# Kernel optimization log

Hardware: AMD Instinct MI355X
Metric: run time of the kernel (lower is better)

Reference implementation:

```python
import jax, jax.numpy as jnp
import numpy as np

B, N, NIN, NHID, D = 8, 2048, 256, 256, 64  # head = 1 (required by squeeze())


def setup_inputs() -> dict:
    key = jax.random.key(0)
    ks = jax.random.split(key, 12)
    xn = lambda k, shape, s=1.0: jax.random.normal(k, shape, jnp.float32) * s
    xav = lambda fi, fo: (2.0 / (fi + fo)) ** 0.5  # xavier_normal std
    return {
        "inputs": xn(ks[0], (B, N, NIN)),
        "fc1_w": xn(ks[1], (NHID, NIN), xav(NIN, NHID)),
        "fc1_b": jnp.full((NHID,), 0.1, jnp.float32),
        "fc2_w": xn(ks[2], (NHID, NHID), xav(NHID, NHID)),
        "fc2_b": jnp.full((NHID,), 0.1, jnp.float32),
        "bn_g": 1.0 + 0.1 * xn(ks[3], (NHID,)),
        "bn_b": 0.1 * xn(ks[4], (NHID,)),
        "bn_mean": 0.1 * xn(ks[5], (NHID,)),
        "bn_var": jax.random.uniform(ks[6], (NHID,), jnp.float32, 0.5, 1.5),
        "wq_w": xn(ks[7], (D, NHID), xav(NHID, D)),
        "wq_b": jnp.full((D,), 0.1, jnp.float32),
        "wk_w": xn(ks[8], (D, NHID), xav(NHID, D)),
        "wk_b": jnp.full((D,), 0.1, jnp.float32),
        "mlp2_w": xn(ks[9], (1, 2 * D), xav(2 * D, 1)),
        "mlp2_b": jnp.full((1,), 0.1, jnp.float32),
    }


def reference(inputs, fc1_w, fc1_b, fc2_w, fc2_b, bn_g, bn_b, bn_mean, bn_var,
              wq_w, wq_b, wk_w, wk_b, mlp2_w, mlp2_b):
    # MLP: Linear -> ELU -> (dropout off, eval) -> Linear -> ELU -> BatchNorm1d (eval, running stats)
    x = jax.nn.elu(jnp.einsum('bni,hi->bnh', inputs, fc1_w) + fc1_b)
    x = jax.nn.elu(jnp.einsum('bnh,oh->bno', x, fc2_w) + fc2_b)
    X = (x - bn_mean) * jax.lax.rsqrt(bn_var + 1e-5) * bn_g + bn_b  # [B,N,NHID]
    # Q/K projections (head=1 -> shapes [B,N,D])
    Xq = jnp.einsum('bnh,dh->bnd', X, wq_w) + wq_b
    Xk = jnp.einsum('bnh,dh->bnd', X, wk_w) + wk_b
    # Original: cat([NK, NQ], -1) over all (i,j) pairs then Linear(2D -> 1).
    # Algebraically identical decomposition: probs[b,i,j] = Xk[b,j].wk_half + Xq[b,i].wq_half + bias
    wk_half, wq_half = mlp2_w[0, :D], mlp2_w[0, D:]
    sk = Xk @ wk_half  # [B,N]  (varies with j, the K/column index)
    sq = Xq @ wq_half  # [B,N]  (varies with i, the Q/row index)
    probs = sq[:, :, None] + sk[:, None, :] + mlp2_b[0]  # [B,N,N]
    return probs
```

## Files before the change

kernel.cpp:

```cpp
#include <hip/hip_runtime.h>
#include <hip/hip_bf16.h>
#include <math.h>

typedef __bf16 bf16x8 __attribute__((ext_vector_type(8)));
typedef float  f32x4  __attribute__((ext_vector_type(4)));
typedef unsigned int u32;
typedef u32 u32x4 __attribute__((ext_vector_type(4)));
typedef unsigned short u16;

#define WS_STG1  0
#define WS_STG2  32768
#define WS_UQ    65536
#define WS_UK    65792
#define WS_CONST 66048
#define WS_SQ    66064
#define WS_SK    82448

__device__ __forceinline__ float elu1(float x) {
    return x > 0.f ? x : (__expf(x) - 1.f);
}

__global__ void prep_all(const float* __restrict__ w1, const float* __restrict__ w2,
                         const float* __restrict__ bn_g, const float* __restrict__ bn_b,
                         const float* __restrict__ bn_mean, const float* __restrict__ bn_var,
                         const float* __restrict__ wq_w, const float* __restrict__ wq_b,
                         const float* __restrict__ wk_w, const float* __restrict__ wk_b,
                         const float* __restrict__ mlp2_w, const float* __restrict__ mlp2_b,
                         float* __restrict__ ws) {
    if (blockIdx.x == 0) {
        __shared__ float redq[256], redk[256];
        const int h = threadIdx.x;
        float s  = bn_g[h] * rsqrtf(bn_var[h] + 1e-5f);
        float tt = bn_b[h] - bn_mean[h] * s;
        float vq = 0.f, vk = 0.f;
        #pragma unroll
        for (int d = 0; d < 64; ++d) {
            vq += wq_w[d * 256 + h] * mlp2_w[64 + d];
            vk += wk_w[d * 256 + h] * mlp2_w[d];
        }
        ws[WS_UQ + h] = s * vq;
        ws[WS_UK + h] = s * vk;
        redq[h] = tt * vq;
        redk[h] = tt * vk;
        __syncthreads();
        for (int st = 128; st > 0; st >>= 1) {
            if (h < st) { redq[h] += redq[h + st]; redk[h] += redk[h + st]; }
            __syncthreads();
        }
        if (h == 0) {
            float cq = 0.f, ck = 0.f;
            for (int d = 0; d < 64; ++d) {
                cq += wq_b[d] * mlp2_w[64 + d];
                ck += wk_b[d] * mlp2_w[d];
            }
            ws[WS_CONST + 0] = redq[0] + cq;
            ws[WS_CONST + 1] = redk[0] + ck;
            ws[WS_CONST + 2] = mlp2_b[0];
        }
        return;
    }
    const int bid = blockIdx.x - 1;
    const int m   = bid >> 3;
    const int kt  = bid & 7;
    const float* src = m ? w2 : w1;
    __bf16* stg = (__bf16*)(ws + (m ? WS_STG2 : WS_STG1));
    const int tid = threadIdx.x;
    #pragma unroll
    for (int it = 0; it < 4; ++it) {
        int idx = it * 256 + tid;
        int nt = idx >> 6, l = idx & 63;
        int lr = l & 15, lk = l >> 4;
        const float* sp = src + (nt * 16 + lr) * 256 + kt * 32 + lk * 8;
        bf16x8 hi;
        #pragma unroll
        for (int j = 0; j < 8; ++j) hi[j] = (__bf16)sp[j];
        *(bf16x8*)(stg + (kt * 16 + nt) * 512 + l * 8) = hi;
    }
}

__global__ __launch_bounds__(256) void main_mfma(const float* __restrict__ inp,
                                                 const float* __restrict__ b1,
                                                 const float* __restrict__ b2,
                                                 float* __restrict__ ws) {
    __shared__ u32 X1p[4096];
    __shared__ float redq[64], redk[64];

    const int tid = threadIdx.x;
    const int l   = tid & 63;
    const int w   = tid >> 6;
    const int lr  = l & 15;
    const int lk  = l >> 4;
    const int rows0 = blockIdx.x * 16;
    const int n0  = w * 64;

    const __bf16* s1 = (const __bf16*)(ws + WS_STG1);
    const __bf16* s2 = (const __bf16*)(ws + WS_STG2);
    const float*  arow = inp + (size_t)(rows0 + lr) * 256 + lk * 8;

    f32x4 acc[4];

    #pragma unroll
    for (int nt = 0; nt < 4; ++nt) acc[nt] = (f32x4)0.f;

    bf16x8 bc[4];
    float4 f0, f1;
    #pragma unroll
    for (int nt = 0; nt < 4; ++nt)
        bc[nt] = *(const bf16x8*)(s1 + ((0 * 16 + w * 4 + nt) << 9) + l * 8);
    f0 = ((const float4*)arow)[0];
    f1 = ((const float4*)arow)[1];

    #pragma unroll
    for (int kt = 0; kt < 8; ++kt) {
        bf16x8 bn[4];
        float4 g0 = f0, g1 = f1;
        if (kt < 7) {
            #pragma unroll
            for (int nt = 0; nt < 4; ++nt)
                bn[nt] = *(const bf16x8*)(s1 + (((kt + 1) * 16 + w * 4 + nt) << 9) + l * 8);
            g0 = ((const float4*)(arow + (kt + 1) * 32))[0];
            g1 = ((const float4*)(arow + (kt + 1) * 32))[1];
        } else {
            #pragma unroll
            for (int nt = 0; nt < 4; ++nt) bn[nt] = bc[nt];
        }
        bf16x8 ah, al;
        {
            float fv[8] = {f0.x,f0.y,f0.z,f0.w,f1.x,f1.y,f1.z,f1.w};
            #pragma unroll
            for (int j = 0; j < 8; ++j) {
                __bf16 hv = (__bf16)fv[j];
                ah[j] = hv;
                al[j] = (__bf16)(fv[j] - (float)hv);
            }
        }
        #pragma unroll
        for (int nt = 0; nt < 4; ++nt) {
            acc[nt] = __builtin_amdgcn_mfma_f32_16x16x32_bf16(ah, bc[nt], acc[nt], 0, 0, 0);
            acc[nt] = __builtin_amdgcn_mfma_f32_16x16x32_bf16(al, bc[nt], acc[nt], 0, 0, 0);
        }
        #pragma unroll
        for (int nt = 0; nt < 4; ++nt) bc[nt] = bn[nt];
        f0 = g0; f1 = g1;
    }
    #pragma unroll
    for (int nt = 0; nt < 4; ++nt) {
        int col = n0 + nt * 16 + lr;
        float bb = b1[col];
        #pragma unroll
        for (int r = 0; r < 4; ++r) {
            int row = lk * 4 + r;
            float v = elu1(acc[nt][r] + bb);
            __bf16 hv = (__bf16)v;
            __bf16 lv = (__bf16)(v - (float)hv);
            u32 pk = ((u32)__builtin_bit_cast(u16, hv) << 16) | __builtin_bit_cast(u16, lv);
            int ob = row * 1024 + ((col * 4) ^ (row << 4));
            *(u32*)((char*)X1p + ob) = pk;
        }
    }
    __syncthreads();

    #pragma unroll
    for (int nt = 0; nt < 4; ++nt) acc[nt] = (f32x4)0.f;

    const int base = lr * 1024;
    const int sw   = lr << 4;

    bf16x8 bc2[4];
    #pragma unroll
    for (int nt = 0; nt < 4; ++nt)
        bc2[nt] = *(const bf16x8*)(s2 + ((0 * 16 + w * 4 + nt) << 9) + l * 8);

    #pragma unroll
    for (int kt = 0; kt < 8; ++kt) {
        bf16x8 bn[4];
        if (kt < 7) {
            #pragma unroll
            for (int nt = 0; nt < 4; ++nt)
                bn[nt] = *(const bf16x8*)(s2 + (((kt + 1) * 16 + w * 4 + nt) << 9) + l * 8);
        } else {
            #pragma unroll
            for (int nt = 0; nt < 4; ++nt) bn[nt] = bc2[nt];
        }
        int cb = kt * 128 + lk * 32;
        u32x4 q0 = *(const u32x4*)((const char*)X1p + base + (cb ^ sw));
        u32x4 q1 = *(const u32x4*)((const char*)X1p + base + ((cb + 16) ^ sw));
        u32 hw0 = __builtin_amdgcn_perm(q0.y, q0.x, 0x07060302u);
        u32 hw1 = __builtin_amdgcn_perm(q0.w, q0.z, 0x07060302u);
        u32 hw2 = __builtin_amdgcn_perm(q1.y, q1.x, 0x07060302u);
        u32 hw3 = __builtin_amdgcn_perm(q1.w, q1.z, 0x07060302u);
        u32 lw0 = __builtin_amdgcn_perm(q0.y, q0.x, 0x05040100u);
        u32 lw1 = __builtin_amdgcn_perm(q0.w, q0.z, 0x05040100u);
        u32 lw2 = __builtin_amdgcn_perm(q1.y, q1.x, 0x05040100u);
        u32 lw3 = __builtin_amdgcn_perm(q1.w, q1.z, 0x05040100u);
        u32x4 hh = {hw0, hw1, hw2, hw3};
        u32x4 ll = {lw0, lw1, lw2, lw3};
        bf16x8 ah = __builtin_bit_cast(bf16x8, hh);
        bf16x8 al = __builtin_bit_cast(bf16x8, ll);
        #pragma unroll
        for (int nt = 0; nt < 4; ++nt) {
            acc[nt] = __builtin_amdgcn_mfma_f32_16x16x32_bf16(ah, bc2[nt], acc[nt], 0, 0, 0);
            acc[nt] = __builtin_amdgcn_mfma_f32_16x16x32_bf16(al, bc2[nt], acc[nt], 0, 0, 0);
        }
        #pragma unroll
        for (int nt = 0; nt < 4; ++nt) bc2[nt] = bn[nt];
    }

    float sqp[4] = {0.f,0.f,0.f,0.f};
    float skp[4] = {0.f,0.f,0.f,0.f};
    const float* uq = ws + WS_UQ;
    const float* uk = ws + WS_UK;
    #pragma unroll
    for (int nt = 0; nt < 4; ++nt) {
        int col = n0 + nt * 16 + lr;
        float bb = b2[col], qc = uq[col], kc = uk[col];
        #pragma unroll
        for (int r = 0; r < 4; ++r) {
            float v = elu1(acc[nt][r] + bb);
            sqp[r] += v * qc;
            skp[r] += v * kc;
        }
    }
    #pragma unroll
    for (int mm = 8; mm >= 1; mm >>= 1) {
        #pragma unroll
        for (int r = 0; r < 4; ++r) {
            sqp[r] += __shfl_xor(sqp[r], mm);
            skp[r] += __shfl_xor(skp[r], mm);
        }
    }
    if (lr == 0) {
        #pragma unroll
        for (int r = 0; r < 4; ++r) {
            int row = lk * 4 + r;
            redq[w * 16 + row] = sqp[r];
            redk[w * 16 + row] = skp[r];
        }
    }
    __syncthreads();
    if (tid < 16) {
        float s = ws[WS_CONST + 0];
        #pragma unroll
        for (int ww = 0; ww < 4; ++ww) s += redq[ww * 16 + tid];
        ws[WS_SQ + rows0 + tid] = s;
    } else if (tid < 32) {
        int rl = tid - 16;
        float s = ws[WS_CONST + 1];
        #pragma unroll
        for (int ww = 0; ww < 4; ++ww) s += redk[ww * 16 + rl];
        ws[WS_SK + rows0 + rl] = s;
    }
}

__global__ __launch_bounds__(256) void broadcast_out(const float* __restrict__ ws,
                                                     float* __restrict__ out) {
    __shared__ float skL[2048];
    const int bi = blockIdx.x;
    const int b = bi >> 8;
    const int chunk = bi & 255;
    const int tid = threadIdx.x;

    float4* skL4 = (float4*)skL;
    const float4* skb4 = (const float4*)(ws + WS_SK + b * 2048);
    #pragma unroll
    for (int it = 0; it < 2; ++it) skL4[it * 256 + tid] = skb4[it * 256 + tid];
    __syncthreads();

    const float mb = ws[WS_CONST + 2];
    const int i0 = chunk * 8;
    #pragma unroll
    for (int i = 0; i < 8; ++i) {
        float sval = ws[WS_SQ + b * 2048 + i0 + i] + mb;
        float4* orow = (float4*)(out + ((size_t)(b * 2048 + i0 + i)) * 2048);
        #pragma unroll
        for (int hh = 0; hh < 2; ++hh) {
            int j4 = hh * 256 + tid;
            float4 v = skL4[j4];
            orow[j4] = make_float4(sval + v.x, sval + v.y, sval + v.z, sval + v.w);
        }
    }
}

extern "C" void kernel_launch(void* const* d_in, const int* in_sizes, int n_in,
                              void* d_out, int out_size, void* d_ws, size_t ws_size,
                              hipStream_t stream) {
    const float* inputs  = (const float*)d_in[0];
    const float* fc1_w   = (const float*)d_in[1];
    const float* fc1_b   = (const float*)d_in[2];
    const float* fc2_w   = (const float*)d_in[3];
    const float* fc2_b   = (const float*)d_in[4];
    const float* bn_g    = (const float*)d_in[5];
    const float* bn_b    = (const float*)d_in[6];
    const float* bn_mean = (const float*)d_in[7];
    const float* bn_var  = (const float*)d_in[8];
    const float* wq_w    = (const float*)d_in[9];
    const float* wq_b    = (const float*)d_in[10];
    const float* wk_w    = (const float*)d_in[11];
    const float* wk_b    = (const float*)d_in[12];
    const float* mlp2_w  = (const float*)d_in[13];
    const float* mlp2_b  = (const float*)d_in[14];
    float* ws  = (float*)d_ws;
    float* out = (float*)d_out;

    hipLaunchKernelGGL(prep_all, dim3(17), dim3(256), 0, stream,
                       fc1_w, fc2_w, bn_g, bn_b, bn_mean, bn_var,
                       wq_w, wq_b, wk_w, wk_b, mlp2_w, mlp2_b, ws);
    hipLaunchKernelGGL(main_mfma, dim3(1024), dim3(256), 0, stream,
                       inputs, fc1_b, fc2_b, ws);
    hipLaunchKernelGGL(broadcast_out, dim3(2048), dim3(256), 0, stream, ws, out);
}
```

Measured before the change: 50.91 us.

## Process 32 rows per block with 8 waves and stagger K-tile start order

Each block of the fused MLP kernel now handles 32 rows using 512 threads, two groups of four waves. Both groups share the same staged weight tiles, so weights can be reused across more rows. The starting K-tile is rotated per block (blockIdx & 7) so concurrent blocks read different weight slices, which spreads L2/cache channel pressure. The trade-off is doubled LDS use (32KB) and fewer, larger blocks (512 instead of 1024), which may reduce scheduling flexibility.

```diff
diff --git a/kernel.cpp b/kernel.cpp
--- a/kernel.cpp
+++ b/kernel.cpp
@@ -78,24 +78,27 @@
     }
 }
 
-__global__ __launch_bounds__(256) void main_mfma(const float* __restrict__ inp,
-                                                 const float* __restrict__ b1,
-                                                 const float* __restrict__ b2,
-                                                 float* __restrict__ ws) {
-    __shared__ u32 X1p[4096];
-    __shared__ float redq[64], redk[64];
+__global__ __launch_bounds__(512, 4) void main_mfma(const float* __restrict__ inp,
+                                                    const float* __restrict__ b1,
+                                                    const float* __restrict__ b2,
+                                                    float* __restrict__ ws) {
+    __shared__ u32 X1p[8192];
+    __shared__ float redq[128], redk[128];
 
     const int tid = threadIdx.x;
     const int l   = tid & 63;
-    const int w   = tid >> 6;
+    const int gw  = tid >> 6;
+    const int w   = gw & 3;
+    const int p   = gw >> 2;
     const int lr  = l & 15;
     const int lk  = l >> 4;
-    const int rows0 = blockIdx.x * 16;
+    const int rows0 = blockIdx.x * 32;
+    const int koff  = blockIdx.x & 7;
     const int n0  = w * 64;
 
     const __bf16* s1 = (const __bf16*)(ws + WS_STG1);
     const __bf16* s2 = (const __bf16*)(ws + WS_STG2);
-    const float*  arow = inp + (size_t)(rows0 + lr) * 256 + lk * 8;
+    const float*  arow = inp + (size_t)(rows0 + p * 16 + lr) * 256 + lk * 8;
 
     f32x4 acc[4];
 
@@ -104,22 +107,26 @@
 
     bf16x8 bc[4];
     float4 f0, f1;
-    #pragma unroll
-    for (int nt = 0; nt < 4; ++nt)
-        bc[nt] = *(const bf16x8*)(s1 + ((0 * 16 + w * 4 + nt) << 9) + l * 8);
-    f0 = ((const float4*)arow)[0];
-    f1 = ((const float4*)arow)[1];
+    {
+        const int kts = koff;
+        #pragma unroll
+        for (int nt = 0; nt < 4; ++nt)
+            bc[nt] = *(const bf16x8*)(s1 + ((kts * 16 + w * 4 + nt) << 9) + l * 8);
+        f0 = ((const float4*)(arow + kts * 32))[0];
+        f1 = ((const float4*)(arow + kts * 32))[1];
+    }
 
     #pragma unroll
     for (int kt = 0; kt < 8; ++kt) {
         bf16x8 bn[4];
         float4 g0 = f0, g1 = f1;
         if (kt < 7) {
+            const int ktn = (kt + 1 + koff) & 7;
             #pragma unroll
             for (int nt = 0; nt < 4; ++nt)
-                bn[nt] = *(const bf16x8*)(s1 + (((kt + 1) * 16 + w * 4 + nt) << 9) + l * 8);
-            g0 = ((const float4*)(arow + (kt + 1) * 32))[0];
-            g1 = ((const float4*)(arow + (kt + 1) * 32))[1];
+                bn[nt] = *(const bf16x8*)(s1 + ((ktn * 16 + w * 4 + nt) << 9) + l * 8);
+            g0 = ((const float4*)(arow + ktn * 32))[0];
+            g1 = ((const float4*)(arow + ktn * 32))[1];
         } else {
             #pragma unroll
             for (int nt = 0; nt < 4; ++nt) bn[nt] = bc[nt];
@@ -149,12 +156,12 @@
         float bb = b1[col];
         #pragma unroll
         for (int r = 0; r < 4; ++r) {
-            int row = lk * 4 + r;
+            int row = p * 16 + lk * 4 + r;
             float v = elu1(acc[nt][r] + bb);
             __bf16 hv = (__bf16)v;
             __bf16 lv = (__bf16)(v - (float)hv);
             u32 pk = ((u32)__builtin_bit_cast(u16, hv) << 16) | __builtin_bit_cast(u16, lv);
-            int ob = row * 1024 + ((col * 4) ^ (row << 4));
+            int ob = row * 1024 + ((col * 4) ^ ((row & 15) << 4));
             *(u32*)((char*)X1p + ob) = pk;
         }
     }
@@ -163,26 +170,28 @@
     #pragma unroll
     for (int nt = 0; nt < 4; ++nt) acc[nt] = (f32x4)0.f;
 
-    const int base = lr * 1024;
+    const int base = (p * 16 + lr) * 1024;
     const int sw   = lr << 4;
 
     bf16x8 bc2[4];
     #pragma unroll
     for (int nt = 0; nt < 4; ++nt)
-        bc2[nt] = *(const bf16x8*)(s2 + ((0 * 16 + w * 4 + nt) << 9) + l * 8);
+        bc2[nt] = *(const bf16x8*)(s2 + ((koff * 16 + w * 4 + nt) << 9) + l * 8);
 
     #pragma unroll
     for (int kt = 0; kt < 8; ++kt) {
+        const int kts = (kt + koff) & 7;
         bf16x8 bn[4];
         if (kt < 7) {
+            const int ktn = (kt + 1 + koff) & 7;
             #pragma unroll
             for (int nt = 0; nt < 4; ++nt)
-                bn[nt] = *(const bf16x8*)(s2 + (((kt + 1) * 16 + w * 4 + nt) << 9) + l * 8);
+                bn[nt] = *(const bf16x8*)(s2 + ((ktn * 16 + w * 4 + nt) << 9) + l * 8);
         } else {
             #pragma unroll
             for (int nt = 0; nt < 4; ++nt) bn[nt] = bc2[nt];
         }
-        int cb = kt * 128 + lk * 32;
+        int cb = kts * 128 + lk * 32;
         u32x4 q0 = *(const u32x4*)((const char*)X1p + base + (cb ^ sw));
         u32x4 q1 = *(const u32x4*)((const char*)X1p + base + ((cb + 16) ^ sw));
         u32 hw0 = __builtin_amdgcn_perm(q0.y, q0.x, 0x07060302u);
@@ -232,23 +241,25 @@
     if (lr == 0) {
         #pragma unroll
         for (int r = 0; r < 4; ++r) {
-            int row = lk * 4 + r;
-            redq[w * 16 + row] = sqp[r];
-            redk[w * 16 + row] = skp[r];
+            int rl = lk * 4 + r;
+            redq[gw * 16 + rl] = sqp[r];
+            redk[gw * 16 + rl] = skp[r];
         }
     }
     __syncthreads();
-    if (tid < 16) {
+    if (tid < 32) {
+        int pp = tid >> 4, rl = tid & 15;
         float s = ws[WS_CONST + 0];
         #pragma unroll
-        for (int ww = 0; ww < 4; ++ww) s += redq[ww * 16 + tid];
+        for (int ww = 0; ww < 4; ++ww) s += redq[(pp * 4 + ww) * 16 + rl];
         ws[WS_SQ + rows0 + tid] = s;
-    } else if (tid < 32) {
-        int rl = tid - 16;
+    } else if (tid < 64) {
+        int rr = tid - 32;
+        int pp = rr >> 4, rl = rr & 15;
         float s = ws[WS_CONST + 1];
         #pragma unroll
-        for (int ww = 0; ww < 4; ++ww) s += redk[ww * 16 + rl];
-        ws[WS_SK + rows0 + rl] = s;
+        for (int ww = 0; ww < 4; ++ww) s += redk[(pp * 4 + ww) * 16 + rl];
+        ws[WS_SK + rows0 + rr] = s;
     }
 }
 
@@ -305,7 +316,7 @@
     hipLaunchKernelGGL(prep_all, dim3(17), dim3(256), 0, stream,
                        fc1_w, fc2_w, bn_g, bn_b, bn_mean, bn_var,
                        wq_w, wq_b, wk_w, wk_b, mlp2_w, mlp2_b, ws);
-    hipLaunchKernelGGL(main_mfma, dim3(1024), dim3(256), 0, stream,
+    hipLaunchKernelGGL(main_mfma, dim3(512), dim3(512), 0, stream,
                        inputs, fc1_b, fc2_b, ws);
     hipLaunchKernelGGL(broadcast_out, dim3(2048), dim3(256), 0, stream, ws, out);
 }
```

Measured after the change: 51.88 us. About the same (+1.9%).
